# Optimization experiments

Hardware: AMD Instinct MI355X
Metric: run time of the kernel (lower is better)

## Reference

```python
import jax, jax.numpy as jnp
import numpy as np

B, L, D = 256, 200, 512


def setup_inputs() -> dict:
    key = jax.random.key(0)
    ks = jax.random.split(key, 13)
    s = 0.04  # ~1/sqrt(D) init scale
    return {
        "session_emb": jax.random.normal(ks[0], (B, L, D), jnp.float32),
        "target_emb": jax.random.normal(ks[1], (B, D), jnp.float32),
        # attention projection (torch.rand in original; scaled for stable softmax)
        "w": jax.random.uniform(ks[2], (D, D), jnp.float32) * s,
        # nn.GRU params (PyTorch layout: weight_ih_l0 [3D, D] in r,z,n order)
        "gru_wih": jax.random.normal(ks[3], (3 * D, D), jnp.float32) * s,
        "gru_whh": jax.random.normal(ks[4], (3 * D, D), jnp.float32) * s,
        "gru_bih": jax.random.normal(ks[5], (3 * D,), jnp.float32) * s,
        "gru_bhh": jax.random.normal(ks[6], (3 * D,), jnp.float32) * s,
        # AUGRUCell: three Linear(2D -> D); input is cat([h_prev, x])
        "reset_w": jax.random.normal(ks[7], (D, 2 * D), jnp.float32) * s,
        "reset_b": jax.random.normal(ks[8], (D,), jnp.float32) * s,
        "update_w": jax.random.normal(ks[9], (D, 2 * D), jnp.float32) * s,
        "update_b": jax.random.normal(ks[10], (D,), jnp.float32) * s,
        "hhat_w": jax.random.normal(ks[11], (D, 2 * D), jnp.float32) * s,
        "hhat_b": jax.random.normal(ks[12], (D,), jnp.float32) * s,
    }


def reference(session_emb, target_emb, w, gru_wih, gru_whh, gru_bih, gru_bhh,
              reset_w, reset_b, update_w, update_b, hhat_w, hhat_b):
    b, l, d = session_emb.shape
    # --- nn.GRU (1 layer, batch_first, h0 = 0). Precompute input projections.
    x_proj = jnp.einsum('bld,ed->ble', session_emb, gru_wih) + gru_bih  # [B,L,3D]

    def gru_step(h, xp):
        hp = h @ gru_whh.T + gru_bhh  # [B,3D]
        xr, xz, xn = jnp.split(xp, 3, axis=-1)
        hr, hz, hn = jnp.split(hp, 3, axis=-1)
        r = jax.nn.sigmoid(xr + hr)
        z = jax.nn.sigmoid(xz + hz)
        n = jnp.tanh(xn + r * hn)
        h_new = (1.0 - z) * n + z * h
        return h_new, h_new

    h0 = jnp.zeros((b, d), session_emb.dtype)
    h_last, s_seq = jax.lax.scan(gru_step, h0, jnp.swapaxes(x_proj, 0, 1))  # s_seq [L,B,D]
    s_state = jnp.swapaxes(s_seq, 0, 1)  # [B,L,D]

    # --- attention = softmax_over_seq( (s_state @ w) @ target ) -> [B,L,1]
    logits = jnp.einsum('bld,de,be->bl', s_state, w, target_emb)
    att = jax.nn.softmax(logits, axis=1)[..., None]  # [B,L,1]

    # --- AUGRU over timesteps, init h = GRU final hidden state
    def augru_step(h, inp):
        x, a = inp  # x: [B,D], a: [B,1]
        ti = jnp.concatenate([h, x], axis=-1)  # cat([h_prev, x])
        r = jax.nn.sigmoid(ti @ reset_w.T + reset_b)
        u = jax.nn.sigmoid(ti @ update_w.T + update_b)
        hh = jnp.tanh(jnp.concatenate([h * r, x], axis=-1) @ hhat_w.T + hhat_b)
        u = a * u
        h_new = (1.0 - u) * h + u * hh
        return h_new, None

    h_final, _ = jax.lax.scan(augru_step, h_last, (s_seq, jnp.swapaxes(att, 0, 1)))
    return h_final
```

## Files before the change

kernel.cpp:

```cpp
#include <hip/hip_runtime.h>
#include <math.h>

#define NL 200
#define SLICE 131072ul

#define BIG_OFF   0ul
#define LG_OFF    26345472ul
#define ATT_OFF   26396672ul
#define VT_OFF    26447872ul
#define HBUF_OFF  26578944ul
#define HR_OFF    26841088ul
#define FLAGS_OFF 26972160ul

__device__ __forceinline__ float sigmoidf_(float x) { return 1.0f / (1.0f + expf(-x)); }

__device__ __forceinline__ float cohld1(const float* p) {
  return __hip_atomic_load(p, __ATOMIC_RELAXED, __HIP_MEMORY_SCOPE_AGENT);
}
__device__ __forceinline__ float2 cohld2(const float* p) {
  union { double d; float2 f; } u;
  u.d = __hip_atomic_load((const double*)p, __ATOMIC_RELAXED, __HIP_MEMORY_SCOPE_AGENT);
  return u.f;
}
__device__ __forceinline__ void cohst1(float* p, float v) {
  __hip_atomic_store(p, v, __ATOMIC_RELAXED, __HIP_MEMORY_SCOPE_AGENT);
}

__device__ __forceinline__ void gwait64(const unsigned* f, unsigned val) {
  const int i = threadIdx.x & 63;
  int guard = 0;
  while (__hip_atomic_load(f + i, __ATOMIC_RELAXED, __HIP_MEMORY_SCOPE_AGENT) < val) {
    if (++guard > (1 << 22)) break;
  }
}
__device__ __forceinline__ void gwait128(const unsigned* f, unsigned val) {
  const int i = threadIdx.x & 63;
  bool d0 = false, d1 = false;
  int guard = 0;
  while (!(d0 && d1)) {
    if (!d0) d0 = __hip_atomic_load(f + i, __ATOMIC_RELAXED, __HIP_MEMORY_SCOPE_AGENT) >= val;
    if (!d1) d1 = __hip_atomic_load(f + i + 64, __ATOMIC_RELAXED, __HIP_MEMORY_SCOPE_AGENT) >= val;
    if (++guard > (1 << 22)) break;
  }
}

__global__ void init_kernel(float* __restrict__ ws) {
  unsigned* const fl = (unsigned*)(ws + FLAGS_OFF);
  for (int j = threadIdx.x; j < 768; j += 256) fl[j] = 0u;
}

__global__ __launch_bounds__(256) void transpose_kernel(const float* __restrict__ in,
                                                        float* __restrict__ ws) {
  __shared__ float tile[64][65];
  const int tx = threadIdx.x & 63, ty = threadIdx.x >> 6;
  const size_t tk0 = (size_t)blockIdx.x * 64;
  const int b0 = blockIdx.y * 64;
#pragma unroll
  for (int r = 0; r < 16; ++r) {
    const int bb = ty + 4 * r;
    tile[bb][tx] = in[(size_t)(b0 + bb) * 102400 + tk0 + tx];
  }
  __syncthreads();
  float* const big1 = ws + BIG_OFF + SLICE;
#pragma unroll
  for (int r = 0; r < 16; ++r) {
    const int kk = ty + 4 * r;
    cohst1(big1 + (tk0 + kk) * 256 + b0 + tx, tile[tx][kk]);
  }
}

__global__ __launch_bounds__(256) void vt_kernel(const float* __restrict__ w,
                                                 const float* __restrict__ tgt,
                                                 float* __restrict__ ws) {
  __shared__ float t_s[512];
  const int b = blockIdx.x, tid = threadIdx.x;
  for (int i = tid; i < 512; i += 256) t_s[i] = tgt[(size_t)b * 512 + i];
  __syncthreads();
  const int wv = tid >> 6, lane = tid & 63;
  for (int d = wv; d < 512; d += 4) {
    const float* const wr = w + (size_t)d * 512;
    const float4 a  = *(const float4*)(wr + lane * 8);
    const float4 a2 = *(const float4*)(wr + lane * 8 + 4);
    float s = a.x * t_s[lane * 8 + 0] + a.y * t_s[lane * 8 + 1] +
              a.z * t_s[lane * 8 + 2] + a.w * t_s[lane * 8 + 3] +
              a2.x * t_s[lane * 8 + 4] + a2.y * t_s[lane * 8 + 5] +
              a2.z * t_s[lane * 8 + 6] + a2.w * t_s[lane * 8 + 7];
    for (int off = 32; off > 0; off >>= 1) s += __shfl_xor(s, off);
    if (lane == 0) ws[VT_OFF + (size_t)d * 256 + b] = s;
  }
}

__global__ __launch_bounds__(512) void gru_kernel(const float* __restrict__ wih,
                                                  const float* __restrict__ whh,
                                                  const float* __restrict__ bih,
                                                  const float* __restrict__ bhh,
                                                  float* __restrict__ ws) {
  __shared__ float wxT[512 * 16];
  __shared__ float whT[512 * 16];
  __shared__ float red[16 * 8 * 130];
  __shared__ float bihs[12], bhhs[12];

  const int bg = blockIdx.x >> 7;
  const int ng = blockIdx.x & 127;
  const int b0 = bg << 7, c0 = ng << 2;
  const int tid = threadIdx.x;

  for (int i = tid; i < 512 * 16; i += 512) {
    const int k = i >> 4, s = i & 15;
    if (s < 12) {
      const int grow = ((s >> 2) << 9) + c0 + (s & 3);
      wxT[i] = wih[(size_t)grow * 512 + k];
      whT[i] = whh[(size_t)grow * 512 + k];
    }
  }
  if (tid < 12) {
    const int grow = ((tid >> 2) << 9) + c0 + (tid & 3);
    bihs[tid] = bih[grow];
    bhhs[tid] = bhh[grow];
  }
  __syncthreads();

  float* const big = ws + BIG_OFF;
  unsigned* const gf = (unsigned*)(ws + FLAGS_OFF) + (bg << 7);

  const int wv = tid >> 6, l = tid & 63;
  const int k0 = wv << 6;
  const int boff = b0 + 2 * l;
  const int qg = tid >> 7;
  const int rr = tid & 127;
  const size_t og = (size_t)(c0 + qg) * 256 + b0 + rr;

  for (int t = 0; t < NL; ++t) {
    const float* const xp = big + (size_t)(t + 1) * SLICE + boff;
    float2 ax[12];
#pragma unroll
    for (int s = 0; s < 12; ++s) ax[s] = make_float2(0.0f, 0.0f);
    for (int bq = 0; bq < 4; ++bq) {
      const int kb = k0 + bq * 16;
      float2 v[16];
#pragma unroll
      for (int j = 0; j < 16; ++j) v[j] = cohld2(xp + (size_t)(kb + j) * 256);
#pragma unroll
      for (int j = 0; j < 16; ++j) {
        const float4* const wr = (const float4*)(wxT + (size_t)(kb + j) * 16);
        float w12[12];
        *(float4*)&w12[0] = wr[0];
        *(float4*)&w12[4] = wr[1];
        *(float4*)&w12[8] = wr[2];
#pragma unroll
        for (int s = 0; s < 12; ++s) {
          ax[s].x += v[j].x * w12[s];
          ax[s].y += v[j].y * w12[s];
        }
      }
    }
    if (t > 0) {
      if (wv == 0) gwait128(gf, (unsigned)t);
      __syncthreads();
    }
    float2 ah[12];
#pragma unroll
    for (int s = 0; s < 12; ++s) ah[s] = make_float2(0.0f, 0.0f);
    float hprev = 0.0f;
    if (t > 0) {
      const float* const hp = big + (size_t)(t - 1) * SLICE + boff;
      hprev = big[(size_t)(t - 1) * SLICE + og];
      for (int bq = 0; bq < 4; ++bq) {
        const int kb = k0 + bq * 16;
        float2 v[16];
#pragma unroll
        for (int j = 0; j < 16; ++j) v[j] = *(const float2*)(hp + (size_t)(kb + j) * 256);
#pragma unroll
        for (int j = 0; j < 16; ++j) {
          const float4* const wr = (const float4*)(whT + (size_t)(kb + j) * 16);
          float w12[12];
          *(float4*)&w12[0] = wr[0];
          *(float4*)&w12[4] = wr[1];
          *(float4*)&w12[8] = wr[2];
#pragma unroll
          for (int s = 0; s < 12; ++s) {
            ah[s].x += v[j].x * w12[s];
            ah[s].y += v[j].y * w12[s];
          }
        }
      }
    }
#pragma unroll
    for (int s = 0; s < 4; ++s) {
      *(float2*)&red[((size_t)(0 + s) * 8 + wv) * 130 + 2 * l] =
          make_float2(ax[s].x + ah[s].x, ax[s].y + ah[s].y);
      *(float2*)&red[((size_t)(4 + s) * 8 + wv) * 130 + 2 * l] =
          make_float2(ax[4 + s].x + ah[4 + s].x, ax[4 + s].y + ah[4 + s].y);
      *(float2*)&red[((size_t)(8 + s) * 8 + wv) * 130 + 2 * l] = ax[8 + s];
      *(float2*)&red[((size_t)(12 + s) * 8 + wv) * 130 + 2 * l] = ah[8 + s];
    }
    __syncthreads();
    float rp = 0, zp = 0, xnp = 0, hnp = 0;
#pragma unroll
    for (int w8 = 0; w8 < 8; ++w8) {
      rp  += red[((size_t)(0 + qg) * 8 + w8) * 130 + rr];
      zp  += red[((size_t)(4 + qg) * 8 + w8) * 130 + rr];
      xnp += red[((size_t)(8 + qg) * 8 + w8) * 130 + rr];
      hnp += red[((size_t)(12 + qg) * 8 + w8) * 130 + rr];
    }
    const float r = sigmoidf_(rp + bihs[0 + qg] + bhhs[0 + qg]);
    const float z = sigmoidf_(zp + bihs[4 + qg] + bhhs[4 + qg]);
    const float n = tanhf(xnp + bihs[8 + qg] + r * (hnp + bhhs[8 + qg]));
    const float hnew = (1.0f - z) * n + z * hprev;
    cohst1(big + (size_t)t * SLICE + og, hnew);
    asm volatile("s_waitcnt vmcnt(0)" ::: "memory");
    __syncthreads();
    if (tid == 0)
      __hip_atomic_store(gf + ng, (unsigned)(t + 1), __ATOMIC_RELAXED, __HIP_MEMORY_SCOPE_AGENT);
  }
}

__global__ __launch_bounds__(256) void attn1_kernel(float* __restrict__ ws) {
  const int l = blockIdx.x, tid = threadIdx.x;
  const float* const sl = ws + BIG_OFF + (size_t)l * SLICE + tid;
  const float* const vtt = ws + VT_OFF + tid;
  float acc = 0.0f;
#pragma unroll 8
  for (int k = 0; k < 512; ++k)
    acc += sl[(size_t)k * 256] * vtt[(size_t)k * 256];
  ws[LG_OFF + (size_t)l * 256 + tid] = acc;
}

__global__ __launch_bounds__(256) void attn2_kernel(float* __restrict__ ws) {
  __shared__ float red[8];
  const int b = blockIdx.x, tid = threadIdx.x;
  const float v = (tid < NL) ? ws[LG_OFF + (size_t)tid * 256 + b] : -3.0e38f;
  float m = v;
  for (int off = 32; off > 0; off >>= 1) m = fmaxf(m, __shfl_xor(m, off));
  if ((tid & 63) == 0) red[tid >> 6] = m;
  __syncthreads();
  m = fmaxf(fmaxf(red[0], red[1]), fmaxf(red[2], red[3]));
  const float e = (tid < NL) ? expf(v - m) : 0.0f;
  float s = e;
  for (int off = 32; off > 0; off >>= 1) s += __shfl_xor(s, off);
  __syncthreads();
  if ((tid & 63) == 0) red[4 + (tid >> 6)] = s;
  __syncthreads();
  s = red[4] + red[5] + red[6] + red[7];
  if (tid < NL) ws[ATT_OFF + (size_t)tid * 256 + b] = e / s;
}

__global__ __launch_bounds__(512) void augru_kernel(const float* __restrict__ rw,
                                                    const float* __restrict__ rbias,
                                                    const float* __restrict__ uw,
                                                    const float* __restrict__ ubias,
                                                    const float* __restrict__ hw,
                                                    const float* __restrict__ hbias,
                                                    float* __restrict__ ws,
                                                    float* __restrict__ out) {
  __shared__ float wT[1024 * 24];
  __shared__ float red[24 * 8 * 66];
  __shared__ float rbs[8], ubs[8], hbs[8];

  const int rg = blockIdx.x >> 6;
  const int cg = blockIdx.x & 63;
  const int r0 = rg << 6, c0 = cg << 3;
  const int tid = threadIdx.x;

  for (int m = 0; m < 3; ++m) {
    const float* const wm = (m == 0) ? rw : (m == 1) ? uw : hw;
    for (int i = tid; i < 8192; i += 512) {
      const int k = i >> 3, c = i & 7;
      wT[(size_t)k * 24 + m * 8 + c] = wm[(size_t)(c0 + c) * 1024 + k];
    }
  }
  if (tid < 8) {
    rbs[tid] = rbias[c0 + tid];
    ubs[tid] = ubias[c0 + tid];
    hbs[tid] = hbias[c0 + tid];
  }
  __syncthreads();

  float* const big = ws + BIG_OFF;
  float* const hbuf = ws + HBUF_OFF;
  float* const hrg = ws + HR_OFF;
  const float* const att = ws + ATT_OFF;
  unsigned* const fbase = (unsigned*)(ws + FLAGS_OFF);
  unsigned* const af1 = fbase + 256 + (rg << 6);
  unsigned* const af2 = fbase + 512 + (rg << 6);

  const int wv = tid >> 6, l = tid & 63;
  const int k0 = wv << 6;
  const int boff = r0 + l;
  const int cq = tid >> 6;
  const int rr = tid & 63;
  const size_t og = (size_t)(c0 + cq) * 256 + r0 + rr;

  for (int t = 0; t < NL; ++t) {
    const float* const xp = big + (size_t)t * SLICE + boff;
    float ax[24];
#pragma unroll
    for (int s = 0; s < 24; ++s) ax[s] = 0.0f;
    for (int bq = 0; bq < 4; ++bq) {
      const int kb = k0 + bq * 16;
      float v[16];
#pragma unroll
      for (int j = 0; j < 16; ++j) v[j] = xp[(size_t)(kb + j) * 256];
#pragma unroll
      for (int j = 0; j < 16; ++j) {
        const float4* const wr = (const float4*)(wT + (size_t)(512 + kb + j) * 24);
        float w24[24];
        *(float4*)&w24[0] = wr[0];  *(float4*)&w24[4] = wr[1];
        *(float4*)&w24[8] = wr[2];  *(float4*)&w24[12] = wr[3];
        *(float4*)&w24[16] = wr[4]; *(float4*)&w24[20] = wr[5];
#pragma unroll
        for (int s = 0; s < 24; ++s) ax[s] += v[j] * w24[s];
      }
    }
    if (t > 0) {
      if (wv == 0) gwait64(af2, (unsigned)t);
      __syncthreads();
    }
    const float* const hsrc = (t == 0) ? (big + 199ul * SLICE) : (hbuf + (size_t)(t & 1) * SLICE);
    const float hcur = cohld1(hsrc + og);
    float ah[16];
#pragma unroll
    for (int s = 0; s < 16; ++s) ah[s] = 0.0f;
    {
      const float* const hp = hsrc + boff;
      for (int bq = 0; bq < 4; ++bq) {
        const int kb = k0 + bq * 16;
        float v[16];
#pragma unroll
        for (int j = 0; j < 16; ++j) v[j] = cohld1(hp + (size_t)(kb + j) * 256);
#pragma unroll
        for (int j = 0; j < 16; ++j) {
          const float4* const wr = (const float4*)(wT + (size_t)(kb + j) * 24);
          float w16[16];
          *(float4*)&w16[0] = wr[0];  *(float4*)&w16[4] = wr[1];
          *(float4*)&w16[8] = wr[2];  *(float4*)&w16[12] = wr[3];
#pragma unroll
          for (int s = 0; s < 16; ++s) ah[s] += v[j] * w16[s];
        }
      }
    }
#pragma unroll
    for (int c = 0; c < 8; ++c) {
      red[((size_t)(0 + c) * 8 + wv) * 66 + l] = ax[c] + ah[c];
      red[((size_t)(8 + c) * 8 + wv) * 66 + l] = ax[8 + c] + ah[8 + c];
      red[((size_t)(16 + c) * 8 + wv) * 66 + l] = ax[16 + c];
    }
    __syncthreads();
    float rp = 0, up = 0, xhp = 0;
#pragma unroll
    for (int w8 = 0; w8 < 8; ++w8) {
      rp  += red[((size_t)(0 + cq) * 8 + w8) * 66 + rr];
      up  += red[((size_t)(8 + cq) * 8 + w8) * 66 + rr];
      xhp += red[((size_t)(16 + cq) * 8 + w8) * 66 + rr];
    }
    const float rgate = sigmoidf_(rp + rbs[cq]);
    const float ug = sigmoidf_(up + ubs[cq]);
    cohst1(hrg + og, rgate * hcur);
    asm volatile("s_waitcnt vmcnt(0)" ::: "memory");
    __syncthreads();
    if (tid == 0)
      __hip_atomic_store(af1 + cg, (unsigned)(t + 1), __ATOMIC_RELAXED, __HIP_MEMORY_SCOPE_AGENT);
    if (wv == 0) gwait64(af1, (unsigned)(t + 1));
    __syncthreads();
    float ahh[8];
#pragma unroll
    for (int s = 0; s < 8; ++s) ahh[s] = 0.0f;
    {
      const float* const rp2 = hrg + boff;
      for (int bq = 0; bq < 4; ++bq) {
        const int kb = k0 + bq * 16;
        float v[16];
#pragma unroll
        for (int j = 0; j < 16; ++j) v[j] = cohld1(rp2 + (size_t)(kb + j) * 256);
#pragma unroll
        for (int j = 0; j < 16; ++j) {
          const float4* const wr = (const float4*)(wT + (size_t)(kb + j) * 24);
          float w8a[8];
          *(float4*)&w8a[0] = wr[4];
          *(float4*)&w8a[4] = wr[5];
#pragma unroll
          for (int s = 0; s < 8; ++s) ahh[s] += v[j] * w8a[s];
        }
      }
    }
#pragma unroll
    for (int c = 0; c < 8; ++c)
      red[((size_t)c * 8 + wv) * 66 + l] = ahh[c];
    __syncthreads();
    float hhp = 0;
#pragma unroll
    for (int w8 = 0; w8 < 8; ++w8)
      hhp += red[((size_t)cq * 8 + w8) * 66 + rr];
    const float hh = tanhf(hhp + xhp + hbs[cq]);
    const float av = att[(size_t)t * 256 + r0 + rr];
    const float u = av * ug;
    const float hn = (1.0f - u) * hcur + u * hh;
    if (t == NL - 1) {
      out[(size_t)(r0 + rr) * 512 + c0 + cq] = hn;
    } else {
      cohst1(hbuf + (size_t)((t + 1) & 1) * SLICE + og, hn);
    }
    asm volatile("s_waitcnt vmcnt(0)" ::: "memory");
    __syncthreads();
    if (tid == 0)
      __hip_atomic_store(af2 + cg, (unsigned)(t + 1), __ATOMIC_RELAXED, __HIP_MEMORY_SCOPE_AGENT);
  }
}

extern "C" void kernel_launch(void* const* d_in, const int* in_sizes, int n_in,
                              void* d_out, int out_size, void* d_ws, size_t ws_size,
                              hipStream_t stream) {
  (void)in_sizes; (void)n_in; (void)out_size; (void)ws_size;
  const float* session = (const float*)d_in[0];
  const float* target  = (const float*)d_in[1];
  const float* w       = (const float*)d_in[2];
  const float* wih     = (const float*)d_in[3];
  const float* whh     = (const float*)d_in[4];
  const float* bih     = (const float*)d_in[5];
  const float* bhh     = (const float*)d_in[6];
  const float* rw      = (const float*)d_in[7];
  const float* rb      = (const float*)d_in[8];
  const float* uw      = (const float*)d_in[9];
  const float* ub      = (const float*)d_in[10];
  const float* hw      = (const float*)d_in[11];
  const float* hb      = (const float*)d_in[12];
  float* ws  = (float*)d_ws;
  float* out = (float*)d_out;

  hipLaunchKernelGGL(init_kernel, dim3(1), dim3(256), 0, stream, ws);
  hipLaunchKernelGGL(transpose_kernel, dim3(1600, 4), dim3(256), 0, stream, session, ws);
  hipLaunchKernelGGL(vt_kernel, dim3(256), dim3(256), 0, stream, w, target, ws);
  hipLaunchKernelGGL(gru_kernel, dim3(256), dim3(512), 0, stream,
                     wih, whh, bih, bhh, ws);
  hipLaunchKernelGGL(attn1_kernel, dim3(200), dim3(256), 0, stream, ws);
  hipLaunchKernelGGL(attn2_kernel, dim3(256), dim3(256), 0, stream, ws);
  hipLaunchKernelGGL(augru_kernel, dim3(256), dim3(512), 0, stream,
                     rw, rb, uw, ub, hw, hb, ws, out);
}
```

Before: 7.192 ms.

## Software-pipeline input projections of next timestep behind the cross-block flag wait

Measured after the change: 11.58 ms. +61.0%, slower.

```diff
diff --git a/kernel.cpp b/kernel.cpp
--- a/kernel.cpp
+++ b/kernel.cpp
@@ -130,11 +130,12 @@
   const int rr = tid & 127;
   const size_t og = (size_t)(c0 + qg) * 256 + b0 + rr;
 
-  for (int t = 0; t < NL; ++t) {
-    const float* const xp = big + (size_t)(t + 1) * SLICE + boff;
-    float2 ax[12];
-#pragma unroll
-    for (int s = 0; s < 12; ++s) ax[s] = make_float2(0.0f, 0.0f);
+  float2 ax[12];
+#pragma unroll
+  for (int s = 0; s < 12; ++s) ax[s] = make_float2(0.0f, 0.0f);
+  {
+    const float* const xp = big + 1ul * SLICE + boff;
+#pragma unroll
     for (int bq = 0; bq < 4; ++bq) {
       const int kb = k0 + bq * 16;
       float2 v[16];
@@ -154,6 +155,9 @@
         }
       }
     }
+  }
+
+  for (int t = 0; t < NL; ++t) {
     if (t > 0) {
       if (wv == 0) gwait128(gf, (unsigned)t);
       __syncthreads();
@@ -165,6 +169,7 @@
     if (t > 0) {
       const float* const hp = big + (size_t)(t - 1) * SLICE + boff;
       hprev = big[(size_t)(t - 1) * SLICE + og];
+#pragma unroll
       for (int bq = 0; bq < 4; ++bq) {
         const int kb = k0 + bq * 16;
         float2 v[16];
@@ -212,6 +217,32 @@
     __syncthreads();
     if (tid == 0)
       __hip_atomic_store(gf + ng, (unsigned)(t + 1), __ATOMIC_RELAXED, __HIP_MEMORY_SCOPE_AGENT);
+    if (t + 1 < NL) {
+      const float* const xp = big + (size_t)(t + 2) * SLICE + boff;
+#pragma unroll
+      for (int s = 0; s < 12; ++s) ax[s] = make_float2(0.0f, 0.0f);
+#pragma unroll
+      for (int bq = 0; bq < 4; ++bq) {
+        const int kb = k0 + bq * 16;
+        float2 v[16];
+#pragma unroll
+        for (int j = 0; j < 16; ++j) v[j] = cohld2(xp + (size_t)(kb + j) * 256);
+#pragma unroll
+        for (int j = 0; j < 16; ++j) {
+          const float4* const wr = (const float4*)(wxT + (size_t)(kb + j) * 16);
+          float w12[12];
+          *(float4*)&w12[0] = wr[0];
+          *(float4*)&w12[4] = wr[1];
+          *(float4*)&w12[8] = wr[2];
+#pragma unroll
+          for (int s = 0; s < 12; ++s) {
+            ax[s].x += v[j].x * w12[s];
+            ax[s].y += v[j].y * w12[s];
+          }
+        }
+      }
+    }
+    asm volatile("" ::: "memory");
   }
 }
 
@@ -291,11 +322,12 @@
   const int rr = tid & 63;
   const size_t og = (size_t)(c0 + cq) * 256 + r0 + rr;
 
-  for (int t = 0; t < NL; ++t) {
-    const float* const xp = big + (size_t)t * SLICE + boff;
-    float ax[24];
-#pragma unroll
-    for (int s = 0; s < 24; ++s) ax[s] = 0.0f;
+  float ax[24];
+#pragma unroll
+  for (int s = 0; s < 24; ++s) ax[s] = 0.0f;
+  {
+    const float* const xp = big + boff;
+#pragma unroll
     for (int bq = 0; bq < 4; ++bq) {
       const int kb = k0 + bq * 16;
       float v[16];
@@ -312,6 +344,9 @@
         for (int s = 0; s < 24; ++s) ax[s] += v[j] * w24[s];
       }
     }
+  }
+
+  for (int t = 0; t < NL; ++t) {
     if (t > 0) {
       if (wv == 0) gwait64(af2, (unsigned)t);
       __syncthreads();
@@ -323,6 +358,7 @@
     for (int s = 0; s < 16; ++s) ah[s] = 0.0f;
     {
       const float* const hp = hsrc + boff;
+#pragma unroll
       for (int bq = 0; bq < 4; ++bq) {
         const int kb = k0 + bq * 16;
         float v[16];
@@ -360,6 +396,29 @@
     __syncthreads();
     if (tid == 0)
       __hip_atomic_store(af1 + cg, (unsigned)(t + 1), __ATOMIC_RELAXED, __HIP_MEMORY_SCOPE_AGENT);
+    if (t + 1 < NL) {
+      const float* const xp = big + (size_t)(t + 1) * SLICE + boff;
+#pragma unroll
+      for (int s = 0; s < 24; ++s) ax[s] = 0.0f;
+#pragma unroll
+      for (int bq = 0; bq < 4; ++bq) {
+        const int kb = k0 + bq * 16;
+        float v[16];
+#pragma unroll
+        for (int j = 0; j < 16; ++j) v[j] = xp[(size_t)(kb + j) * 256];
+#pragma unroll
+        for (int j = 0; j < 16; ++j) {
+          const float4* const wr = (const float4*)(wT + (size_t)(512 + kb + j) * 24);
+          float w24[24];
+          *(float4*)&w24[0] = wr[0];  *(float4*)&w24[4] = wr[1];
+          *(float4*)&w24[8] = wr[2];  *(float4*)&w24[12] = wr[3];
+          *(float4*)&w24[16] = wr[4]; *(float4*)&w24[20] = wr[5];
+#pragma unroll
+          for (int s = 0; s < 24; ++s) ax[s] += v[j] * w24[s];
+        }
+      }
+    }
+    asm volatile("" ::: "memory");
     if (wv == 0) gwait64(af1, (unsigned)(t + 1));
     __syncthreads();
     float ahh[8];
@@ -367,6 +426,7 @@
     for (int s = 0; s < 8; ++s) ahh[s] = 0.0f;
     {
       const float* const rp2 = hrg + boff;
+#pragma unroll
       for (int bq = 0; bq < 4; ++bq) {
         const int kb = k0 + bq * 16;
         float v[16];
```
